# Kernel tuning notes

Hardware: AMD Instinct MI355X
Metric: run time of the kernel (lower is better)

The kernel has to match this reference:

```python
import jax, jax.numpy as jnp
import numpy as np

B, S, H = 2, 2048, 2048
NH, NKV, HD = 32, 8, 64          # num_heads, num_kv_heads, head_dim
G = NH // NKV                     # GQA group size
NEG = -1e9


def setup_inputs() -> dict:
    key = jax.random.key(0)
    ks = jax.random.split(key, 8)
    x = jax.random.normal(ks[0], (B, S, H), dtype=jnp.float32)
    # real RoPE frequencies: theta = 10000 ** (-2i/hd)
    inv_freq = 1.0 / (10000.0 ** (np.arange(0, HD, 2, dtype=np.float32) / HD))
    angles = np.arange(S, dtype=np.float32)[:, None] * inv_freq[None, :]  # [S, HD//2]
    freqs_cos = jnp.asarray(np.cos(angles))
    freqs_sin = jnp.asarray(np.sin(angles))
    # additive causal mask [S, S]
    mask = jnp.where(jnp.tril(jnp.ones((S, S), dtype=bool)), 0.0, NEG).astype(jnp.float32)
    sc = 0.02
    Wq = jax.random.normal(ks[1], (NH * HD, H), dtype=jnp.float32) * sc
    bq = jax.random.normal(ks[2], (NH * HD,), dtype=jnp.float32) * sc
    Wk = jax.random.normal(ks[3], (NKV * HD, H), dtype=jnp.float32) * sc
    bk = jax.random.normal(ks[4], (NKV * HD,), dtype=jnp.float32) * sc
    Wv = jax.random.normal(ks[5], (NKV * HD, H), dtype=jnp.float32) * sc
    bv = jax.random.normal(ks[6], (NKV * HD,), dtype=jnp.float32) * sc
    Wo = jax.random.normal(ks[7], (H, NH * HD), dtype=jnp.float32) * sc
    return {"x": x, "freqs_cos": freqs_cos, "freqs_sin": freqs_sin, "mask": mask,
            "Wq": Wq, "bq": bq, "Wk": Wk, "bk": bk, "Wv": Wv, "bv": bv, "Wo": Wo}


def _rotate_half(t):
    h = t.shape[-1] // 2
    return jnp.concatenate([-t[..., h:], t[..., :h]], axis=-1)


def reference(x, freqs_cos, freqs_sin, mask, Wq, bq, Wk, bk, Wv, bv, Wo):
    b, s, _ = x.shape
    q = (x @ Wq.T + bq).reshape(b, s, NH, HD)
    k = (x @ Wk.T + bk).reshape(b, s, NKV, HD)
    v = (x @ Wv.T + bv).reshape(b, s, NKV, HD)
    # RoPE (rotate_half style): cos/sin duplicated along last dim -> [1, s, 1, HD]
    cos = jnp.concatenate([freqs_cos, freqs_cos], axis=-1)[None, :, None, :]
    sin = jnp.concatenate([freqs_sin, freqs_sin], axis=-1)[None, :, None, :]
    q = q * cos + _rotate_half(q) * sin
    k = k * cos + _rotate_half(k) * sin
    # GQA: view q as [b, s, NKV, G, HD]; avoids repeat_interleave of K/V (same math)
    q5 = q.reshape(b, s, NKV, G, HD)
    scores = jnp.einsum('bqhgd,bkhd->bhgqk', q5, k) / jnp.sqrt(jnp.float32(HD))
    scores = scores + mask  # broadcast [s, s] over [b, h, g, s, s]
    p = jax.nn.softmax(scores.astype(jnp.float32), axis=-1).astype(q.dtype)
    out = jnp.einsum('bhgqk,bkhd->bqhgd', p, v).reshape(b, s, NH * HD)
    return out @ Wo.T
```

## Files before the change

### kernel.cpp

```cpp
#include <hip/hip_runtime.h>
#include <hip/hip_bf16.h>
#include <cstddef>
#include <cstdint>

#define B_   2
#define S_   2048
#define H_   2048
#define NH_  32
#define NKV_ 8
#define HD_  64

typedef __attribute__((ext_vector_type(8))) short short8;
typedef __attribute__((ext_vector_type(4))) float v4f;
typedef __attribute__((ext_vector_type(16))) float v16f;

#define MAXC 48.0f
#define QSCALE 0.18033688011112042f

__device__ __forceinline__ unsigned short f2b(float f) {
    unsigned int u = __float_as_uint(f);
    u += 0x7FFFu + ((u >> 16) & 1u);
    return (unsigned short)(u >> 16);
}
__device__ __forceinline__ unsigned int pkbf(float a, float b) {
    __hip_bfloat162 h = __float22bfloat162_rn(float2{a, b});
    return *(unsigned int*)&h;
}
__device__ __forceinline__ float fexp2(float x) {
#if __has_builtin(__builtin_amdgcn_exp2f)
    return __builtin_amdgcn_exp2f(x);
#else
    return exp2f(x);
#endif
}
__device__ __forceinline__ v4f mfma16(short8 a, short8 b, v4f c) {
    return __builtin_amdgcn_mfma_f32_16x16x32_bf16(a, b, c, 0, 0, 0);
}
__device__ __forceinline__ v16f mfma32(short8 a, short8 b, v16f c) {
    return __builtin_amdgcn_mfma_f32_32x32x16_bf16(a, b, c, 0, 0, 0);
}
__device__ __forceinline__ void gll16(void* lds, const void* g) {
    __builtin_amdgcn_global_load_lds(
        (const __attribute__((address_space(1))) unsigned int*)g,
        (__attribute__((address_space(3))) unsigned int*)lds, 16, 0, 0);
}

__global__ __launch_bounds__(256) void convert_all(
    const float* __restrict__ x, const float* __restrict__ wq,
    const float* __restrict__ wk, const float* __restrict__ wv,
    const float* __restrict__ wo,
    unsigned short* __restrict__ xb, unsigned short* __restrict__ wqb,
    unsigned short* __restrict__ wkb, unsigned short* __restrict__ wvb,
    unsigned short* __restrict__ wob)
{
    size_t i = ((size_t)blockIdx.x * 256 + threadIdx.x) * 4;
    const float* src; unsigned short* dst; size_t off;
    if (i < 8388608)       { src = x;  dst = xb;  off = i; }
    else if (i < 12582912) { src = wq; dst = wqb; off = i - 8388608; }
    else if (i < 13631488) { src = wk; dst = wkb; off = i - 12582912; }
    else if (i < 14680064) { src = wv; dst = wvb; off = i - 13631488; }
    else                   { src = wo; dst = wob; off = i - 14680064; }
    float4 v = *(const float4*)(src + off);
    ushort4 o;
    o.x = f2b(v.x); o.y = f2b(v.y); o.z = f2b(v.z); o.w = f2b(v.w);
    *(ushort4*)(dst + off) = o;
}


#define STG_A(c, i, t) gll16(&As[c][(w * 32 + (i) * 8) * 64], \
                             ga + (size_t)((i) * 8) * 2048 + (size_t)(t) * 64);
#define STG_B(c, i, t) gll16(&Bs[c][(w * 16 + (i) * 8) * 64], \
                             gb + (size_t)((i) * 8) * 2048 + (size_t)(t) * 64);

__global__ __launch_bounds__(512, 2) void qkv_gemm(
    const unsigned short* __restrict__ xb,
    const unsigned short* __restrict__ wqb, const unsigned short* __restrict__ wkb,
    const unsigned short* __restrict__ wvb,
    const float* __restrict__ bq, const float* __restrict__ bk,
    const float* __restrict__ bv,
    const float* __restrict__ fc, const float* __restrict__ fs,
    unsigned short* __restrict__ Qb, unsigned short* __restrict__ Kb,
    unsigned short* __restrict__ Vt)
{
    __shared__ unsigned short As[3][256 * 64];
    __shared__ unsigned short Bs[3][128 * 64];
    const int tid = threadIdx.x;
    const int lane = tid & 63, w = tid >> 6;
    const int tx = lane & 15, quad = lane >> 4;

    const int bid = blockIdx.x;
    const int swz = (bid & 7) * 48 + (bid >> 3);
    const int bi = swz / 24, bj = swz % 24;
    const int bm = bi * 256;

    const unsigned short* Bp; int mode, nbase;
    if (bj < 16)      { Bp = wqb + (size_t)(bj * 128) * 2048;        mode = 0; nbase = bj * 128; }
    else if (bj < 20) { Bp = wkb + (size_t)((bj - 16) * 128) * 2048; mode = 1; nbase = (bj - 16) * 128; }
    else              { Bp = wvb + (size_t)((bj - 20) * 128) * 2048; mode = 2; nbase = (bj - 20) * 128; }
    const unsigned short* Ap = xb + (size_t)bm * 2048;

    const int wm = (w >> 1) * 64, wn = (w & 1) * 64;

    v4f acc[4][4];
#pragma unroll
    for (int i = 0; i < 4; ++i)
#pragma unroll
        for (int j = 0; j < 4; ++j) acc[i][j] = (v4f)0.f;

    const int r8 = lane >> 3, gc = (lane & 7) ^ r8;
    const unsigned short* ga = Ap + (size_t)(w * 32 + r8) * 2048 + gc * 8;
    const unsigned short* gb = Bp + (size_t)(w * 16 + r8) * 2048 + gc * 8;

    const int t7 = tx & 7;
    int sl[2];
#pragma unroll
    for (int kk = 0; kk < 2; ++kk) sl[kk] = ((kk * 4 + quad) ^ t7) * 8;

    STG_A(0, 0, 0) STG_A(0, 1, 0) STG_B(0, 0, 0)
    STG_A(0, 2, 0) STG_A(0, 3, 0) STG_B(0, 1, 0)
    STG_A(1, 0, 1) STG_A(1, 1, 1) STG_B(1, 0, 1)
    STG_A(1, 2, 1) STG_A(1, 3, 1) STG_B(1, 1, 1)

    int cb = 0;
    for (int t = 0; t < 32; ++t) {
        if (t < 31) asm volatile("s_waitcnt vmcnt(6)" ::: "memory");
        else        asm volatile("s_waitcnt vmcnt(0)" ::: "memory");
        __builtin_amdgcn_sched_barrier(0);
        __builtin_amdgcn_s_barrier();
        __builtin_amdgcn_sched_barrier(0);

        const unsigned short* Asb = As[cb];
        const unsigned short* Bsb = Bs[cb];
        const int nb = (cb == 0) ? 2 : cb - 1;
        const bool pf = (t < 30);

        short8 af[4][2], bf[2][2];
#pragma unroll
        for (int mt = 0; mt < 4; ++mt)
#pragma unroll
            for (int kk = 0; kk < 2; ++kk)
                af[mt][kk] = *(const short8*)&Asb[(wm + mt * 16 + tx) * 64 + sl[kk]];
#pragma unroll
        for (int nt = 0; nt < 2; ++nt)
#pragma unroll
            for (int kk = 0; kk < 2; ++kk)
                bf[nt][kk] = *(const short8*)&Bsb[(wn + nt * 16 + tx) * 64 + sl[kk]];
        if (pf) { STG_A(nb, 0, t + 2) STG_A(nb, 1, t + 2) STG_B(nb, 0, t + 2) }
        __builtin_amdgcn_s_setprio(1);
#pragma unroll
        for (int kk = 0; kk < 2; ++kk)
#pragma unroll
            for (int mt = 0; mt < 4; ++mt)
#pragma unroll
                for (int nt = 0; nt < 2; ++nt)
                    acc[mt][nt] = mfma16(af[mt][kk], bf[nt][kk], acc[mt][nt]);
        __builtin_amdgcn_s_setprio(0);
        __builtin_amdgcn_sched_barrier(0);
        __builtin_amdgcn_s_barrier();
        __builtin_amdgcn_sched_barrier(0);

#pragma unroll
        for (int nt = 0; nt < 2; ++nt)
#pragma unroll
            for (int kk = 0; kk < 2; ++kk)
                bf[nt][kk] = *(const short8*)&Bsb[(wn + (nt + 2) * 16 + tx) * 64 + sl[kk]];
        if (pf) { STG_A(nb, 2, t + 2) STG_A(nb, 3, t + 2) STG_B(nb, 1, t + 2) }
        __builtin_amdgcn_s_setprio(1);
#pragma unroll
        for (int kk = 0; kk < 2; ++kk)
#pragma unroll
            for (int mt = 0; mt < 4; ++mt)
#pragma unroll
                for (int nt = 0; nt < 2; ++nt)
                    acc[mt][nt + 2] = mfma16(af[mt][kk], bf[nt][kk], acc[mt][nt + 2]);
        __builtin_amdgcn_s_setprio(0);
        cb = (cb == 2) ? 0 : cb + 1;
    }

    if (mode <= 1) {
        unsigned short* Cout = mode ? Kb : Qb;
        const float* bias    = mode ? bk : bq;
        const int ldN        = mode ? 512 : 2048;
        const float scq      = mode ? 1.0f : QSCALE;
        float bx0 = bias[nbase + wn +  0 + tx];
        float bx1 = bias[nbase + wn + 16 + tx];
        float bx2 = bias[nbase + wn + 32 + tx];
        float bx3 = bias[nbase + wn + 48 + tx];
#pragma unroll
        for (int mt = 0; mt < 4; ++mt)
#pragma unroll
            for (int rg = 0; rg < 4; ++rg) {
                int m = bm + wm + mt * 16 + quad * 4 + rg;
                int s = m & (S_ - 1);
                float c0 = fc[s * 32 + tx],      c1 = fc[s * 32 + 16 + tx];
                float s0 = fs[s * 32 + tx],      s1 = fs[s * 32 + 16 + tx];
                float q0 = acc[mt][0][rg] + bx0, q1 = acc[mt][1][rg] + bx1;
                float q2 = acc[mt][2][rg] + bx2, q3 = acc[mt][3][rg] + bx3;
                size_t base = (size_t)m * ldN + nbase + wn + tx;
                Cout[base]      = f2b((q0 * c0 - q2 * s0) * scq);
                Cout[base + 16] = f2b((q1 * c1 - q3 * s1) * scq);
                Cout[base + 32] = f2b((q2 * c0 + q0 * s0) * scq);
                Cout[base + 48] = f2b((q3 * c1 + q1 * s1) * scq);
            }
    } else {
#pragma unroll
        for (int nt = 0; nt < 4; ++nt) {
            int d = nbase + wn + nt * 16 + tx;
            float bvv = bv[d];
#pragma unroll
            for (int mt = 0; mt < 4; ++mt) {
                int m0 = bm + wm + mt * 16 + quad * 4;
                ushort4 o;
                o.x = f2b(acc[mt][nt][0] + bvv);
                o.y = f2b(acc[mt][nt][1] + bvv);
                o.z = f2b(acc[mt][nt][2] + bvv);
                o.w = f2b(acc[mt][nt][3] + bvv);
                *(ushort4*)&Vt[(size_t)d * 4096 + m0] = o;
            }
        }
    }
}

__global__ __launch_bounds__(512, 2) void out_gemm(
    const unsigned short* __restrict__ Ab, const unsigned short* __restrict__ Bw,
    float* __restrict__ C)
{
    __shared__ unsigned short As[3][256 * 64];
    __shared__ unsigned short Bs[3][128 * 64];
    const int tid = threadIdx.x;
    const int lane = tid & 63, w = tid >> 6;
    const int tx = lane & 15, quad = lane >> 4;

    const int bid = blockIdx.x;
    const int swz = (bid & 7) * 32 + (bid >> 3);
    const int bm = (swz >> 4) * 256, bn = (swz & 15) * 128;

    const int wm = (w >> 1) * 64, wn = (w & 1) * 64;

    v4f acc[4][4];
#pragma unroll
    for (int i = 0; i < 4; ++i)
#pragma unroll
        for (int j = 0; j < 4; ++j) acc[i][j] = (v4f)0.f;

    const int r8 = lane >> 3, gc = (lane & 7) ^ r8;
    const unsigned short* ga = Ab + (size_t)(bm + w * 32 + r8) * 2048 + gc * 8;
    const unsigned short* gb = Bw + (size_t)(bn + w * 16 + r8) * 2048 + gc * 8;

    const int t7 = tx & 7;
    int sl[2];
#pragma unroll
    for (int kk = 0; kk < 2; ++kk) sl[kk] = ((kk * 4 + quad) ^ t7) * 8;

    STG_A(0, 0, 0) STG_A(0, 1, 0) STG_B(0, 0, 0)
    STG_A(0, 2, 0) STG_A(0, 3, 0) STG_B(0, 1, 0)
    STG_A(1, 0, 1) STG_A(1, 1, 1) STG_B(1, 0, 1)
    STG_A(1, 2, 1) STG_A(1, 3, 1) STG_B(1, 1, 1)

    int cb = 0;
    for (int t = 0; t < 32; ++t) {
        if (t < 31) asm volatile("s_waitcnt vmcnt(6)" ::: "memory");
        else        asm volatile("s_waitcnt vmcnt(0)" ::: "memory");
        __builtin_amdgcn_sched_barrier(0);
        __builtin_amdgcn_s_barrier();
        __builtin_amdgcn_sched_barrier(0);

        const unsigned short* Asb = As[cb];
        const unsigned short* Bsb = Bs[cb];
        const int nb = (cb == 0) ? 2 : cb - 1;
        const bool pf = (t < 30);

        short8 af[4][2], bf[2][2];
#pragma unroll
        for (int mt = 0; mt < 4; ++mt)
#pragma unroll
            for (int kk = 0; kk < 2; ++kk)
                af[mt][kk] = *(const short8*)&Asb[(wm + mt * 16 + tx) * 64 + sl[kk]];
#pragma unroll
        for (int nt = 0; nt < 2; ++nt)
#pragma unroll
            for (int kk = 0; kk < 2; ++kk)
                bf[nt][kk] = *(const short8*)&Bsb[(wn + nt * 16 + tx) * 64 + sl[kk]];
        if (pf) { STG_A(nb, 0, t + 2) STG_A(nb, 1, t + 2) STG_B(nb, 0, t + 2) }
        __builtin_amdgcn_s_setprio(1);
#pragma unroll
        for (int kk = 0; kk < 2; ++kk)
#pragma unroll
            for (int mt = 0; mt < 4; ++mt)
#pragma unroll
                for (int nt = 0; nt < 2; ++nt)
                    acc[mt][nt] = mfma16(af[mt][kk], bf[nt][kk], acc[mt][nt]);
        __builtin_amdgcn_s_setprio(0);
        __builtin_amdgcn_sched_barrier(0);
        __builtin_amdgcn_s_barrier();
        __builtin_amdgcn_sched_barrier(0);

#pragma unroll
        for (int nt = 0; nt < 2; ++nt)
#pragma unroll
            for (int kk = 0; kk < 2; ++kk)
                bf[nt][kk] = *(const short8*)&Bsb[(wn + (nt + 2) * 16 + tx) * 64 + sl[kk]];
        if (pf) { STG_A(nb, 2, t + 2) STG_A(nb, 3, t + 2) STG_B(nb, 1, t + 2) }
        __builtin_amdgcn_s_setprio(1);
#pragma unroll
        for (int kk = 0; kk < 2; ++kk)
#pragma unroll
            for (int mt = 0; mt < 4; ++mt)
#pragma unroll
                for (int nt = 0; nt < 2; ++nt)
                    acc[mt][nt + 2] = mfma16(af[mt][kk], bf[nt][kk], acc[mt][nt + 2]);
        __builtin_amdgcn_s_setprio(0);
        cb = (cb == 2) ? 0 : cb + 1;
    }

#pragma unroll
    for (int mt = 0; mt < 4; ++mt)
#pragma unroll
        for (int nt = 0; nt < 4; ++nt)
#pragma unroll
            for (int rg = 0; rg < 4; ++rg) {
                int m = bm + wm + mt * 16 + quad * 4 + rg;
                C[(size_t)m * 2048 + bn + wn + nt * 16 + tx] = acc[mt][nt][rg];
            }
}

__global__ __launch_bounds__(256, 4) void attn_mfma(
    const unsigned short* __restrict__ Q, const unsigned short* __restrict__ K,
    const unsigned short* __restrict__ Vt, unsigned short* __restrict__ O)
{
    __shared__ __align__(16) unsigned short smem[2][2][64 * 72];
    const int tid = threadIdx.x;
    const int lane = tid & 63, wq = tid >> 6;
    const int l32 = lane & 31, half = lane >> 5;
    const int qh = wq & 1;
    const int ts = wq >> 1;
    const int p = blockIdx.x;
    const int h = blockIdx.y, b = blockIdx.z;
    const int kvh = h >> 2;

    const int srow = tid >> 3, sc8 = (tid & 7) * 8;
    const unsigned short* gkB = &K[(((size_t)b * S_ + srow) * NKV_ + kvh) * HD_ + sc8];
    const unsigned short* gvB = &Vt[(size_t)(kvh * 64 + srow) * 4096 + (size_t)b * 2048 + sc8];
    const int woff = srow * 72 + sc8;

    for (int ph = 0; ph < 2; ++ph) {
        const int T = ph ? (31 - p) : p;

        const int qrow = T * 64 + qh * 32 + l32;
        const unsigned short* Qr = &Q[(((size_t)b * S_ + qrow) * NH_ + h) * HD_];
        short8 qf[4];
#pragma unroll
        for (int s = 0; s < 4; ++s)
            qf[s] = *(const short8*)(Qr + s * 16 + half * 8);

        float la = 0.f, lb = 0.f, lc = 0.f, ld = 0.f;
        v16f o0 = (v16f)0.f, o1 = (v16f)0.f;

        uint4 kr0 = *(const uint4*)(gkB);
        uint4 kr1 = *(const uint4*)(gkB + 32 * (NKV_ * HD_));
        uint4 vr0 = *(const uint4*)(gvB);
        uint4 vr1 = *(const uint4*)(gvB + (size_t)32 * 4096);
        int cur = 0;

        for (int kt = 0; kt <= T; ++kt) {
            unsigned short* Kw = &smem[cur][0][woff];
            unsigned short* Vw = &smem[cur][1][woff];
            *(uint4*)(Kw)           = kr0;
            *(uint4*)(Kw + 32 * 72) = kr1;
            *(uint4*)(Vw)           = vr0;
            *(uint4*)(Vw + 32 * 72) = vr1;
            __syncthreads();
            if (kt < T) {
                const unsigned short* gk = gkB + (size_t)(kt + 1) * 64 * (NKV_ * HD_);
                const unsigned short* gv = gvB + (kt + 1) * 64;
                kr0 = *(const uint4*)(gk);
                kr1 = *(const uint4*)(gk + 32 * (NKV_ * HD_));
                vr0 = *(const uint4*)(gv);
                vr1 = *(const uint4*)(gv + (size_t)32 * 4096);
            }
            const unsigned short* Ksb = smem[cur][0];
            const unsigned short* Vsb = smem[cur][1];
            cur ^= 1;

            const bool diag = (kt == T);
            if (diag && ts > qh) continue;
            const bool part = diag && (ts == qh);

            const int kb = (ts * 32 + l32) * 72 + half * 8;
            v16f st = (v16f)(-MAXC);
            __builtin_amdgcn_s_setprio(1);
            st = mfma32(*(const short8*)&Ksb[kb],      qf[0], st);
            st = mfma32(*(const short8*)&Ksb[kb + 16], qf[1], st);
            st = mfma32(*(const short8*)&Ksb[kb + 32], qf[2], st);
            st = mfma32(*(const short8*)&Ksb[kb + 48], qf[3], st);
            __builtin_amdgcn_s_setprio(0);

            float pv[16];
#pragma unroll
            for (int r = 0; r < 16; ++r) pv[r] = fexp2(st[r]);
            if (part) {
#pragma unroll
                for (int r = 0; r < 16; ++r) {
                    int krow = (r & 3) + 8 * (r >> 2) + 4 * half;
                    if (krow > l32) pv[r] = 0.f;
                }
            }
            la += (pv[0]  + pv[1])  + (pv[2]  + pv[3]);
            lb += (pv[4]  + pv[5])  + (pv[6]  + pv[7]);
            lc += (pv[8]  + pv[9])  + (pv[10] + pv[11]);
            ld += (pv[12] + pv[13]) + (pv[14] + pv[15]);

            unsigned int u[8];
#pragma unroll
            for (int g = 0; g < 4; ++g) {
                u[2 * g]     = pkbf(pv[4 * g],     pv[4 * g + 1]);
                u[2 * g + 1] = pkbf(pv[4 * g + 2], pv[4 * g + 3]);
            }
#pragma unroll
            for (int sg = 0; sg < 2; ++sg) {
                unsigned int a0 = u[4 * sg], a1 = u[4 * sg + 1];
                unsigned int b0 = u[4 * sg + 2], b1 = u[4 * sg + 3];
                uint4 fw;
#if __has_builtin(__builtin_amdgcn_permlane32_swap)
                typedef unsigned int u2v __attribute__((ext_vector_type(2)));
                u2v r0 = __builtin_amdgcn_permlane32_swap(a0, b0, false, false);
                u2v r1 = __builtin_amdgcn_permlane32_swap(a1, b1, false, false);
                fw.x = r0[0]; fw.y = r1[0]; fw.z = r0[1]; fw.w = r1[1];
#else
                unsigned int s0 = __shfl_xor((int)a0, 32);
                unsigned int s1 = __shfl_xor((int)a1, 32);
                unsigned int s2 = __shfl_xor((int)b0, 32);
                unsigned int s3 = __shfl_xor((int)b1, 32);
                fw.x = half ? s2 : a0;
                fw.y = half ? s3 : a1;
                fw.z = half ? b0 : s0;
                fw.w = half ? b1 : s1;
#endif
                short8 pf = *(short8*)&fw;
                const int vo = (2 * ts + sg) * 16 + half * 8;
                __builtin_amdgcn_s_setprio(1);
                o0 = mfma32(*(const short8*)&Vsb[l32 * 72 + vo],        pf, o0);
                o1 = mfma32(*(const short8*)&Vsb[(32 + l32) * 72 + vo], pf, o1);
                __builtin_amdgcn_s_setprio(0);
            }
        }

        float l = (la + lb) + (lc + ld);
        l += __shfl_xor(l, 32);

        __syncthreads();
        float* red = (float*)&smem[0][0][0];
        const int rbase = (qh * 64 + lane) * 33;
        if (ts == 1) {
#pragma unroll
            for (int r = 0; r < 16; ++r) { red[rbase + r] = o0[r]; red[rbase + 16 + r] = o1[r]; }
            red[rbase + 32] = l;
        }
        __syncthreads();
        if (ts == 0) {
#pragma unroll
            for (int r = 0; r < 16; ++r) { o0[r] += red[rbase + r]; o1[r] += red[rbase + 16 + r]; }
            l += red[rbase + 32];
            float inv = 1.f / l;
            int qg = T * 64 + qh * 32 + l32;
            unsigned short* orow = &O[((size_t)b * S_ + qg) * (NH_ * HD_) + h * HD_];
#pragma unroll
            for (int td = 0; td < 2; ++td) {
                const v16f& oo = td ? o1 : o0;
#pragma unroll
                for (int g = 0; g < 4; ++g) {
                    int d = td * 32 + g * 8 + half * 4;
                    uint2 uu;
                    uu.x = pkbf(oo[4 * g] * inv,     oo[4 * g + 1] * inv);
                    uu.y = pkbf(oo[4 * g + 2] * inv, oo[4 * g + 3] * inv);
                    *(uint2*)&orow[d] = uu;
                }
            }
        }
        if (ph == 0) __syncthreads();
    }
}

extern "C" void kernel_launch(void* const* d_in, const int* in_sizes, int n_in,
                              void* d_out, int out_size, void* d_ws, size_t ws_size,
                              hipStream_t stream)
{
    const float* x  = (const float*)d_in[0];
    const float* fc = (const float*)d_in[1];
    const float* fs = (const float*)d_in[2];
    const float* Wq = (const float*)d_in[4];
    const float* bq = (const float*)d_in[5];
    const float* Wk = (const float*)d_in[6];
    const float* bk = (const float*)d_in[7];
    const float* Wv = (const float*)d_in[8];
    const float* bv = (const float*)d_in[9];
    const float* Wo = (const float*)d_in[10];
    float* out = (float*)d_out;

    unsigned short* ws = (unsigned short*)d_ws;
    unsigned short* xb  = ws;
    unsigned short* wqb = ws + 8388608;
    unsigned short* wkb = ws + 12582912;
    unsigned short* wvb = ws + 13631488;
    unsigned short* wob = ws + 14680064;
    unsigned short* Qb  = ws + 18874368;
    unsigned short* Kb  = ws + 27262976;
    unsigned short* Vt  = ws + 29360128;
    unsigned short* Ob  = ws + 31457280;

    dim3 blk(256);
    convert_all<<<18432, blk, 0, stream>>>(x, Wq, Wk, Wv, Wo, xb, wqb, wkb, wvb, wob);
    qkv_gemm<<<384, dim3(512), 0, stream>>>(xb, wqb, wkb, wvb, bq, bk, bv,
                                            fc, fs, Qb, Kb, Vt);
    attn_mfma<<<dim3(16, NH_, B_), blk, 0, stream>>>(Qb, Kb, Vt, Ob);
    out_gemm<<<256, dim3(512), 0, stream>>>(Ob, wob, out);
}
```

Baseline: 298.3 us.

## Enlarge QKV GEMM tile to 256x256 with double-buffered LDS pipeline

The QKV projection GEMM moves from 256x128 tiles with a triple-buffered LDS ring to 256x256 tiles with double buffering, so each wave computes a 128x64 sub-tile in four MFMA phases, and the grid shrinks from 384 to 192 blocks. The larger tile raises arithmetic intensity and halves redundant reads of x. In exchange it doubles the accumulator registers, which risks losing two-blocks-per-CU occupancy. The prefetch depth also drops from two tiles to one with a full vmcnt(0) wait each iteration, which can expose load latency, and 192 blocks may underfill the GPU's compute units.

```diff
diff --git a/kernel.cpp b/kernel.cpp
--- a/kernel.cpp
+++ b/kernel.cpp
@@ -66,12 +66,6 @@
     *(ushort4*)(dst + off) = o;
 }
 
-
-#define STG_A(c, i, t) gll16(&As[c][(w * 32 + (i) * 8) * 64], \
-                             ga + (size_t)((i) * 8) * 2048 + (size_t)(t) * 64);
-#define STG_B(c, i, t) gll16(&Bs[c][(w * 16 + (i) * 8) * 64], \
-                             gb + (size_t)((i) * 8) * 2048 + (size_t)(t) * 64);
-
 __global__ __launch_bounds__(512, 2) void qkv_gemm(
     const unsigned short* __restrict__ xb,
     const unsigned short* __restrict__ wqb, const unsigned short* __restrict__ wkb,
@@ -82,59 +76,60 @@
     unsigned short* __restrict__ Qb, unsigned short* __restrict__ Kb,
     unsigned short* __restrict__ Vt)
 {
-    __shared__ unsigned short As[3][256 * 64];
-    __shared__ unsigned short Bs[3][128 * 64];
+    __shared__ unsigned short As[2][256 * 64];
+    __shared__ unsigned short Bs[2][256 * 64];
     const int tid = threadIdx.x;
     const int lane = tid & 63, w = tid >> 6;
     const int tx = lane & 15, quad = lane >> 4;
 
     const int bid = blockIdx.x;
-    const int swz = (bid & 7) * 48 + (bid >> 3);
-    const int bi = swz / 24, bj = swz % 24;
+    const int swz = (bid & 7) * 24 + (bid >> 3);
+    const int bi = swz / 12, bj = swz % 12;
     const int bm = bi * 256;
 
     const unsigned short* Bp; int mode, nbase;
-    if (bj < 16)      { Bp = wqb + (size_t)(bj * 128) * 2048;        mode = 0; nbase = bj * 128; }
-    else if (bj < 20) { Bp = wkb + (size_t)((bj - 16) * 128) * 2048; mode = 1; nbase = (bj - 16) * 128; }
-    else              { Bp = wvb + (size_t)((bj - 20) * 128) * 2048; mode = 2; nbase = (bj - 20) * 128; }
+    if (bj < 8)       { Bp = wqb + (size_t)(bj * 256) * 2048;        mode = 0; nbase = bj * 256; }
+    else if (bj < 10) { Bp = wkb + (size_t)((bj - 8) * 256) * 2048;  mode = 1; nbase = (bj - 8) * 256; }
+    else              { Bp = wvb + (size_t)((bj - 10) * 256) * 2048; mode = 2; nbase = (bj - 10) * 256; }
     const unsigned short* Ap = xb + (size_t)bm * 2048;
 
-    const int wm = (w >> 1) * 64, wn = (w & 1) * 64;
-
-    v4f acc[4][4];
-#pragma unroll
-    for (int i = 0; i < 4; ++i)
+    const int wm = (w >> 2) * 128, wn = (w & 3) * 64;
+
+    v4f acc[8][4];
+#pragma unroll
+    for (int i = 0; i < 8; ++i)
 #pragma unroll
         for (int j = 0; j < 4; ++j) acc[i][j] = (v4f)0.f;
 
     const int r8 = lane >> 3, gc = (lane & 7) ^ r8;
     const unsigned short* ga = Ap + (size_t)(w * 32 + r8) * 2048 + gc * 8;
-    const unsigned short* gb = Bp + (size_t)(w * 16 + r8) * 2048 + gc * 8;
+    const unsigned short* gb = Bp + (size_t)(w * 32 + r8) * 2048 + gc * 8;
+
+#define SA(c, i, t) gll16(&As[c][(w * 32 + (i) * 8) * 64], \
+                          ga + (size_t)((i) * 8) * 2048 + (size_t)(t) * 64);
+#define SB(c, i, t) gll16(&Bs[c][(w * 32 + (i) * 8) * 64], \
+                          gb + (size_t)((i) * 8) * 2048 + (size_t)(t) * 64);
 
     const int t7 = tx & 7;
     int sl[2];
 #pragma unroll
     for (int kk = 0; kk < 2; ++kk) sl[kk] = ((kk * 4 + quad) ^ t7) * 8;
 
-    STG_A(0, 0, 0) STG_A(0, 1, 0) STG_B(0, 0, 0)
-    STG_A(0, 2, 0) STG_A(0, 3, 0) STG_B(0, 1, 0)
-    STG_A(1, 0, 1) STG_A(1, 1, 1) STG_B(1, 0, 1)
-    STG_A(1, 2, 1) STG_A(1, 3, 1) STG_B(1, 1, 1)
-
-    int cb = 0;
+    SA(0, 0, 0) SA(0, 1, 0) SA(0, 2, 0) SA(0, 3, 0)
+    SB(0, 0, 0) SB(0, 1, 0) SB(0, 2, 0) SB(0, 3, 0)
+
+    short8 af[4][2], bf[2][2];
+
     for (int t = 0; t < 32; ++t) {
-        if (t < 31) asm volatile("s_waitcnt vmcnt(6)" ::: "memory");
-        else        asm volatile("s_waitcnt vmcnt(0)" ::: "memory");
+        const int cur = t & 1, nxt = cur ^ 1;
+        asm volatile("s_waitcnt vmcnt(0)" ::: "memory");
         __builtin_amdgcn_sched_barrier(0);
         __builtin_amdgcn_s_barrier();
         __builtin_amdgcn_sched_barrier(0);
-
-        const unsigned short* Asb = As[cb];
-        const unsigned short* Bsb = Bs[cb];
-        const int nb = (cb == 0) ? 2 : cb - 1;
-        const bool pf = (t < 30);
-
-        short8 af[4][2], bf[2][2];
+        const unsigned short* Asb = As[cur];
+        const unsigned short* Bsb = Bs[cur];
+        const bool pf = (t < 31);
+
 #pragma unroll
         for (int mt = 0; mt < 4; ++mt)
 #pragma unroll
@@ -145,7 +140,7 @@
 #pragma unroll
             for (int kk = 0; kk < 2; ++kk)
                 bf[nt][kk] = *(const short8*)&Bsb[(wn + nt * 16 + tx) * 64 + sl[kk]];
-        if (pf) { STG_A(nb, 0, t + 2) STG_A(nb, 1, t + 2) STG_B(nb, 0, t + 2) }
+        if (pf) { SA(nxt, 0, t + 1) SA(nxt, 1, t + 1) }
         __builtin_amdgcn_s_setprio(1);
 #pragma unroll
         for (int kk = 0; kk < 2; ++kk)
@@ -164,7 +159,7 @@
 #pragma unroll
             for (int kk = 0; kk < 2; ++kk)
                 bf[nt][kk] = *(const short8*)&Bsb[(wn + (nt + 2) * 16 + tx) * 64 + sl[kk]];
-        if (pf) { STG_A(nb, 2, t + 2) STG_A(nb, 3, t + 2) STG_B(nb, 1, t + 2) }
+        if (pf) { SA(nxt, 2, t + 1) SA(nxt, 3, t + 1) }
         __builtin_amdgcn_s_setprio(1);
 #pragma unroll
         for (int kk = 0; kk < 2; ++kk)
@@ -174,8 +169,47 @@
                 for (int nt = 0; nt < 2; ++nt)
                     acc[mt][nt + 2] = mfma16(af[mt][kk], bf[nt][kk], acc[mt][nt + 2]);
         __builtin_amdgcn_s_setprio(0);
-        cb = (cb == 2) ? 0 : cb + 1;
+        __builtin_amdgcn_sched_barrier(0);
+        __builtin_amdgcn_s_barrier();
+        __builtin_amdgcn_sched_barrier(0);
+
+#pragma unroll
+        for (int mt = 0; mt < 4; ++mt)
+#pragma unroll
+            for (int kk = 0; kk < 2; ++kk)
+                af[mt][kk] = *(const short8*)&Asb[(wm + 64 + mt * 16 + tx) * 64 + sl[kk]];
+        if (pf) { SB(nxt, 0, t + 1) SB(nxt, 1, t + 1) }
+        __builtin_amdgcn_s_setprio(1);
+#pragma unroll
+        for (int kk = 0; kk < 2; ++kk)
+#pragma unroll
+            for (int mt = 0; mt < 4; ++mt)
+#pragma unroll
+                for (int nt = 0; nt < 2; ++nt)
+                    acc[mt + 4][nt + 2] = mfma16(af[mt][kk], bf[nt][kk], acc[mt + 4][nt + 2]);
+        __builtin_amdgcn_s_setprio(0);
+        __builtin_amdgcn_sched_barrier(0);
+        __builtin_amdgcn_s_barrier();
+        __builtin_amdgcn_sched_barrier(0);
+
+#pragma unroll
+        for (int nt = 0; nt < 2; ++nt)
+#pragma unroll
+            for (int kk = 0; kk < 2; ++kk)
+                bf[nt][kk] = *(const short8*)&Bsb[(wn + nt * 16 + tx) * 64 + sl[kk]];
+        if (pf) { SB(nxt, 2, t + 1) SB(nxt, 3, t + 1) }
+        __builtin_amdgcn_s_setprio(1);
+#pragma unroll
+        for (int kk = 0; kk < 2; ++kk)
+#pragma unroll
+            for (int mt = 0; mt < 4; ++mt)
+#pragma unroll
+                for (int nt = 0; nt < 2; ++nt)
+                    acc[mt + 4][nt] = mfma16(af[mt][kk], bf[nt][kk], acc[mt + 4][nt]);
+        __builtin_amdgcn_s_setprio(0);
     }
+#undef SA
+#undef SB
 
     if (mode <= 1) {
         unsigned short* Cout = mode ? Kb : Qb;
@@ -187,7 +221,7 @@
         float bx2 = bias[nbase + wn + 32 + tx];
         float bx3 = bias[nbase + wn + 48 + tx];
 #pragma unroll
-        for (int mt = 0; mt < 4; ++mt)
+        for (int mt = 0; mt < 8; ++mt)
 #pragma unroll
             for (int rg = 0; rg < 4; ++rg) {
                 int m = bm + wm + mt * 16 + quad * 4 + rg;
@@ -208,7 +242,7 @@
             int d = nbase + wn + nt * 16 + tx;
             float bvv = bv[d];
 #pragma unroll
-            for (int mt = 0; mt < 4; ++mt) {
+            for (int mt = 0; mt < 8; ++mt) {
                 int m0 = bm + wm + mt * 16 + quad * 4;
                 ushort4 o;
                 o.x = f2b(acc[mt][nt][0] + bvv);
@@ -220,6 +254,11 @@
         }
     }
 }
+
+#define STG_A(c, i, t) gll16(&As[c][(w * 32 + (i) * 8) * 64], \
+                             ga + (size_t)((i) * 8) * 2048 + (size_t)(t) * 64);
+#define STG_B(c, i, t) gll16(&Bs[c][(w * 16 + (i) * 8) * 64], \
+                             gb + (size_t)((i) * 8) * 2048 + (size_t)(t) * 64);
 
 __global__ __launch_bounds__(512, 2) void out_gemm(
     const unsigned short* __restrict__ Ab, const unsigned short* __restrict__ Bw,
@@ -510,7 +549,7 @@
 
     dim3 blk(256);
     convert_all<<<18432, blk, 0, stream>>>(x, Wq, Wk, Wv, Wo, xb, wqb, wkb, wvb, wob);
-    qkv_gemm<<<384, dim3(512), 0, stream>>>(xb, wqb, wkb, wvb, bq, bk, bv,
+    qkv_gemm<<<192, dim3(512), 0, stream>>>(xb, wqb, wkb, wvb, bq, bk, bv,
                                             fc, fs, Qb, Kb, Vt);
     attn_mfma<<<dim3(16, NH_, B_), blk, 0, stream>>>(Qb, Kb, Vt, Ob);
     out_gemm<<<256, dim3(512), 0, stream>>>(Ob, wob, out);
```

New measurement: 303.2 us. Within noise of the previous version (+1.6%).
